# Kernel optimization log

Measured on AMD Instinct MI355X. Metric: run time of the kernel, lower is better.

## Reference

```python
import jax, jax.numpy as jnp
import numpy as np

EPS = 1e-6

def setup_inputs() -> dict:
    key = jax.random.key(0)
    k1, k2, k3, k4 = jax.random.split(key, 4)
    B, N, E, C_in, C_out = 8, 4096, 2048, 128, 128
    x = jax.random.normal(k1, (B, N, C_in), dtype=jnp.float32)
    H = jax.random.uniform(k2, (B, N, E), dtype=jnp.float32)
    # nn.Linear(in_ch, out_ch): W is [out_ch, in_ch], b is [out_ch]
    W = jax.random.normal(k3, (C_out, C_in), dtype=jnp.float32) / np.sqrt(C_in)
    b = jax.random.normal(k4, (C_out,), dtype=jnp.float32) * 0.01
    return {"x": x, "H": H, "W": W, "b": b}

def reference(x, H, W, b):
    # Degree normalizers (diag_embed + bmm in original == broadcast row scale)
    De = jnp.sum(H, axis=1) + EPS          # [B, E] hyperedge degrees
    Dv = jnp.sum(H, axis=2) + EPS          # [B, N] node degrees
    inv_sqrt_Dv = 1.0 / jnp.sqrt(Dv)       # [B, N]
    out = x * inv_sqrt_Dv[..., None]                 # Dv^{-1/2} x
    out = jnp.einsum('bne,bnc->bec', H, out)         # H^T (..)
    out = out / De[..., None]                        # De^{-1} (..)
    out = jnp.einsum('bne,bec->bnc', H, out)         # H (..)
    out = out * inv_sqrt_Dv[..., None]               # Dv^{-1/2} (..)
    return out @ W.T + b                             # Linear
```

## Files before the change

### kernel.cpp

```cpp
#include <hip/hip_runtime.h>


#define EPS 1e-6f
constexpr int B_ = 8, N_ = 4096, E_ = 2048, C_ = 128;

typedef __bf16 bf16x8 __attribute__((ext_vector_type(8)));
typedef float f32x4 __attribute__((ext_vector_type(4)));

__device__ __forceinline__ unsigned int f2bf_pack(float lo, float hi) {
  unsigned int ul = __float_as_uint(lo), uh = __float_as_uint(hi);
  ul = (ul + 0x7fffu + ((ul >> 16) & 1u)) >> 16;
  uh = (uh + 0x7fffu + ((uh >> 16) & 1u)) & 0xffff0000u;
  return uh | ul;
}

__device__ __forceinline__ void gl2lds16(const void* g, void* l) {
  __builtin_amdgcn_global_load_lds(
      (const __attribute__((address_space(1))) void*)g,
      (__attribute__((address_space(3))) void*)l, 16, 0, 0);
}

__global__ __launch_bounds__(256) void k1a_cast_dv(
    const float* __restrict__ H, unsigned short* __restrict__ Hbf,
    float* __restrict__ Dv) {
  const int t = threadIdx.x;
  const int w = t >> 6, l = t & 63;
  const size_t row = (size_t)blockIdx.x * 4 + w;
  const float* src = H + row * E_;
  unsigned short* dst = Hbf + row * E_;
  float s = 0.f;
#pragma unroll
  for (int i = 0; i < 8; ++i) {
    const f32x4 v = *(const f32x4*)(src + 256 * i + 4 * l);
    s += v[0] + v[1] + v[2] + v[3];
    uint2 p;
    p.x = f2bf_pack(v[0], v[1]);
    p.y = f2bf_pack(v[2], v[3]);
    *(uint2*)(dst + 256 * i + 4 * l) = p;
  }
#pragma unroll
  for (int o = 32; o; o >>= 1) s += __shfl_xor(s, o);
  if (l == 0) Dv[row] = s;
}

__global__ __launch_bounds__(256) void k1b_transpose_de(
    const unsigned short* __restrict__ Hbf, unsigned short* __restrict__ HT,
    float* __restrict__ De) {
  __shared__ unsigned int T[128][66];
  const int t = threadIdx.x;
  const int b = blockIdx.z;
  const int n0 = blockIdx.x * 128, e0 = blockIdx.y * 128;
  const int q = t >> 2, cq = t & 3;
  const unsigned short* r0p = Hbf + ((size_t)b * N_ + n0 + 2 * q) * E_ + e0;
  const unsigned short* r1p = r0p + E_;
#pragma unroll
  for (int i = 0; i < 8; ++i) {
    const int c = 16 * i + 4 * cq;
    const uint2 a = *(const uint2*)(r0p + c);
    const uint2 bb = *(const uint2*)(r1p + c);
    T[c + 0][q] = (a.x & 0xffffu) | (bb.x << 16);
    T[c + 1][q] = (a.x >> 16) | (bb.x & 0xffff0000u);
    T[c + 2][q] = (a.y & 0xffffu) | (bb.y << 16);
    T[c + 3][q] = (a.y >> 16) | (bb.y & 0xffff0000u);
  }
  __syncthreads();
  const int crow = t >> 1, h = t & 1;
  unsigned int u[32];
  float s = 0.f;
#pragma unroll
  for (int i = 0; i < 32; ++i) {
    u[i] = T[crow][h * 32 + i];
    s += __uint_as_float(u[i] << 16) + __uint_as_float(u[i] & 0xffff0000u);
  }
  uint4* dst = (uint4*)(HT + ((size_t)b * E_ + e0 + crow) * N_ + n0 + 64 * h);
#pragma unroll
  for (int i = 0; i < 8; ++i)
    dst[i] = make_uint4(u[4 * i], u[4 * i + 1], u[4 * i + 2], u[4 * i + 3]);
  s += __shfl_xor(s, 1);
  if (h == 0) atomicAdd(&De[b * E_ + e0 + crow], s);
}

__global__ __launch_bounds__(256) void st0_scale_transpose(
    const float* __restrict__ in, const float* __restrict__ deg,
    unsigned short* __restrict__ outT) {
  __shared__ unsigned int T[128][66];
  const int t = threadIdx.x;
  in += (size_t)blockIdx.y * N_ * 128;
  outT += (size_t)blockIdx.y * 128 * N_;
  deg += (size_t)blockIdx.y * N_;
  const int r0 = blockIdx.x * 128;
  const int q = t >> 2, cq = t & 3;
  const float* row0 = in + (size_t)(r0 + 2 * q) * 128;
  const float* row1 = row0 + 128;
  const float s0 = 1.f / sqrtf(deg[r0 + 2 * q] + EPS);
  const float s1 = 1.f / sqrtf(deg[r0 + 2 * q + 1] + EPS);
#pragma unroll
  for (int i = 0; i < 8; ++i) {
    const int c = 16 * i + 4 * cq;
    const f32x4 a = *(const f32x4*)(row0 + c);
    const f32x4 b2 = *(const f32x4*)(row1 + c);
#pragma unroll
    for (int j = 0; j < 4; ++j) T[c + j][q] = f2bf_pack(a[j] * s0, b2[j] * s1);
  }
  __syncthreads();
  const int crow = t >> 1, h = t & 1;
  unsigned int u[32];
#pragma unroll
  for (int i = 0; i < 32; ++i) u[i] = T[crow][h * 32 + i];
  uint4* dst = (uint4*)(outT + (size_t)crow * N_ + r0 + 64 * h);
#pragma unroll
  for (int i = 0; i < 8; ++i)
    dst[i] = make_uint4(u[4 * i], u[4 * i + 1], u[4 * i + 2], u[4 * i + 3]);
}

__global__ __launch_bounds__(256) void st1_sum(
    const float* __restrict__ p0, const float* __restrict__ p1,
    const float* __restrict__ De, unsigned short* __restrict__ out2T) {
  __shared__ unsigned int T[128][66];
  const int t = threadIdx.x;
  const int b = blockIdx.y;
  const int r0 = blockIdx.x * 128;
  const int q = t >> 2, cq = t & 3;
  const size_t base = ((size_t)b * E_ + r0 + 2 * q) * C_;
  const float s0 = 1.f / (De[b * E_ + r0 + 2 * q] + EPS);
  const float s1 = 1.f / (De[b * E_ + r0 + 2 * q + 1] + EPS);
#pragma unroll
  for (int i = 0; i < 8; ++i) {
    const int c = 16 * i + 4 * cq;
    const f32x4 a = *(const f32x4*)(p0 + base + c);
    const f32x4 a1 = *(const f32x4*)(p1 + base + c);
    const f32x4 bb = *(const f32x4*)(p0 + base + C_ + c);
    const f32x4 b1 = *(const f32x4*)(p1 + base + C_ + c);
#pragma unroll
    for (int j = 0; j < 4; ++j)
      T[c + j][q] = f2bf_pack((a[j] + a1[j]) * s0, (bb[j] + b1[j]) * s1);
  }
  __syncthreads();
  const int crow = t >> 1, h = t & 1;
  unsigned int u[32];
#pragma unroll
  for (int i = 0; i < 32; ++i) u[i] = T[crow][h * 32 + i];
  uint4* dst = (uint4*)(out2T + ((size_t)b * C_ + crow) * E_ + r0 + 64 * h);
#pragma unroll
  for (int i = 0; i < 8; ++i)
    dst[i] = make_uint4(u[4 * i], u[4 * i + 1], u[4 * i + 2], u[4 * i + 3]);
}

__global__ __launch_bounds__(256) void gemm_bt_splitk(
    const unsigned short* __restrict__ A, const unsigned short* __restrict__ Bt,
    float* __restrict__ C0, float* __restrict__ C1, int M, int Kfull, int Kper) {
  __shared__ unsigned short Als[128 * 32];
  __shared__ unsigned short Bls[128 * 32];
  const int t = threadIdx.x;
  const int w = t >> 6, l = t & 63;
  const int mt = blockIdx.x, sk = blockIdx.y, b = blockIdx.z;
  const unsigned short* Ab = A + ((size_t)b * M + mt * 128) * Kfull + (size_t)sk * Kper;
  const unsigned short* Btb = Bt + (size_t)b * 128 * Kfull + (size_t)sk * Kper;
  const int srow = l >> 2, scol = (l & 3) * 8;
  const unsigned short* ga0 = Ab + (size_t)(w * 32 + srow) * Kfull + scol;
  const unsigned short* ga1 = ga0 + (size_t)16 * Kfull;
  const unsigned short* gb0 = Btb + (size_t)(w * 32 + srow) * Kfull + scol;
  const unsigned short* gb1 = gb0 + (size_t)16 * Kfull;
  unsigned short* const la0 = Als + (w * 32) * 32;
  unsigned short* const la1 = Als + (w * 32 + 16) * 32;
  unsigned short* const lb0 = Bls + (w * 32) * 32;
  unsigned short* const lb1 = Bls + (w * 32 + 16) * 32;
  const int mrow = (w & 1) * 64, ncol = (w >> 1) * 64;
  const int fr = l & 15, fq = l >> 4;
  f32x4 acc[4][4];
#pragma unroll
  for (int i = 0; i < 4; ++i)
#pragma unroll
    for (int j = 0; j < 4; ++j) acc[i][j] = (f32x4){0.f, 0.f, 0.f, 0.f};
  const int nsteps = Kper / 32;
  for (int kt = 0; kt < nsteps; ++kt) {
    __syncthreads();
    gl2lds16(ga0, la0);
    gl2lds16(ga1, la1);
    gl2lds16(gb0, lb0);
    gl2lds16(gb1, lb1);
    ga0 += 32; ga1 += 32; gb0 += 32; gb1 += 32;
    __syncthreads();
    bf16x8 af[4], bfr[4];
#pragma unroll
    for (int i = 0; i < 4; ++i) {
      af[i] = *(const bf16x8*)(Als + (mrow + i * 16 + fr) * 32 + fq * 8);
      bfr[i] = *(const bf16x8*)(Bls + (ncol + i * 16 + fr) * 32 + fq * 8);
    }
#pragma unroll
    for (int i = 0; i < 4; ++i)
#pragma unroll
      for (int j = 0; j < 4; ++j)
        acc[i][j] = __builtin_amdgcn_mfma_f32_16x16x32_bf16(af[i], bfr[j], acc[i][j], 0, 0, 0);
  }
  float* Cb = (sk == 0 ? C0 : C1) + ((size_t)b * M + mt * 128) * 128;
#pragma unroll
  for (int i = 0; i < 4; ++i)
#pragma unroll
    for (int j = 0; j < 4; ++j)
#pragma unroll
      for (int r = 0; r < 4; ++r) {
        const int row = mrow + i * 16 + fq * 4 + r;
        const int col = ncol + j * 16 + fr;
        Cb[(size_t)row * 128 + col] = acc[i][j][r];
      }
}

__global__ __launch_bounds__(256) void k5_linear(
    float* __restrict__ io, const float* __restrict__ q1,
    const float* __restrict__ W, const float* __restrict__ bias,
    const float* __restrict__ Dv) {
  __shared__ unsigned short Als[128 * 136];
  __shared__ unsigned short Wls[128 * 136];
  const int t = threadIdx.x;
  const size_t r0 = (size_t)blockIdx.x * 128;
  {
    const int row = t >> 1, h = t & 1;
    const float* src0 = io + (r0 + row) * 128 + h * 64;
    const float* src1 = q1 + (r0 + row) * 128 + h * 64;
    const float sc = 1.f / sqrtf(Dv[r0 + row] + EPS);
    unsigned short* ld = Als + row * 136 + h * 64;
    const float* wsrc = W + row * 128 + h * 64;
    unsigned short* lw = Wls + row * 136 + h * 64;
#pragma unroll
    for (int i = 0; i < 16; ++i) {
      const f32x4 a = *(const f32x4*)(src0 + 4 * i);
      const f32x4 a1 = *(const f32x4*)(src1 + 4 * i);
      uint2 p;
      p.x = f2bf_pack((a[0] + a1[0]) * sc, (a[1] + a1[1]) * sc);
      p.y = f2bf_pack((a[2] + a1[2]) * sc, (a[3] + a1[3]) * sc);
      *(uint2*)(ld + 4 * i) = p;
      const f32x4 ww = *(const f32x4*)(wsrc + 4 * i);
      uint2 pw;
      pw.x = f2bf_pack(ww[0], ww[1]);
      pw.y = f2bf_pack(ww[2], ww[3]);
      *(uint2*)(lw + 4 * i) = pw;
    }
  }
  __syncthreads();
  const int w = t >> 6, l = t & 63;
  const int mrow = (w & 1) * 64, ncol = (w >> 1) * 64;
  const int fr = l & 15, fq = l >> 4;
  f32x4 acc[4][4];
#pragma unroll
  for (int i = 0; i < 4; ++i)
#pragma unroll
    for (int j = 0; j < 4; ++j) acc[i][j] = (f32x4){0.f, 0.f, 0.f, 0.f};
#pragma unroll
  for (int s = 0; s < 4; ++s) {
    bf16x8 af[4], bfr[4];
#pragma unroll
    for (int i = 0; i < 4; ++i) {
      af[i] = *(const bf16x8*)(Als + (mrow + i * 16 + fr) * 136 + s * 32 + fq * 8);
      bfr[i] = *(const bf16x8*)(Wls + (ncol + i * 16 + fr) * 136 + s * 32 + fq * 8);
    }
#pragma unroll
    for (int i = 0; i < 4; ++i)
#pragma unroll
      for (int j = 0; j < 4; ++j)
        acc[i][j] = __builtin_amdgcn_mfma_f32_16x16x32_bf16(af[i], bfr[j], acc[i][j], 0, 0, 0);
  }
#pragma unroll
  for (int i = 0; i < 4; ++i)
#pragma unroll
    for (int j = 0; j < 4; ++j)
#pragma unroll
      for (int r = 0; r < 4; ++r) {
        const int row = mrow + i * 16 + fq * 4 + r;
        const int col = ncol + j * 16 + fr;
        io[(r0 + row) * 128 + col] = acc[i][j][r] + bias[col];
      }
}

extern "C" void kernel_launch(void* const* d_in, const int* in_sizes, int n_in,
                              void* d_out, int out_size, void* d_ws, size_t ws_size,
                              hipStream_t stream) {
  const float* x = (const float*)d_in[0];
  const float* H = (const float*)d_in[1];
  const float* W = (const float*)d_in[2];
  const float* bias = (const float*)d_in[3];
  float* out = (float*)d_out;

  unsigned short* Hbf = (unsigned short*)d_ws;
  unsigned short* HT = Hbf + (size_t)B_ * N_ * E_;
  unsigned short* xsT = HT + (size_t)B_ * N_ * E_;
  unsigned short* out2T = xsT + (size_t)B_ * C_ * N_;
  float* Dv = (float*)(out2T + (size_t)B_ * C_ * E_);
  float* De = Dv + B_ * N_;

  float* g1p0 = out;
  float* g1p1 = out + (size_t)B_ * E_ * C_;
  float* g2p1 = (float*)HT;

  hipMemsetAsync(De, 0, (size_t)B_ * E_ * sizeof(float), stream);

  k1a_cast_dv<<<dim3(B_ * N_ / 4), 256, 0, stream>>>(H, Hbf, Dv);
  k1b_transpose_de<<<dim3(N_ / 128, E_ / 128, B_), 256, 0, stream>>>(Hbf, HT, De);
  st0_scale_transpose<<<dim3(N_ / 128, B_), 256, 0, stream>>>(x, Dv, xsT);
  gemm_bt_splitk<<<dim3(E_ / 128, 2, B_), 256, 0, stream>>>(HT, xsT, g1p0, g1p1, E_, N_, N_ / 2);
  st1_sum<<<dim3(E_ / 128, B_), 256, 0, stream>>>(g1p0, g1p1, De, out2T);
  gemm_bt_splitk<<<dim3(N_ / 128, 2, B_), 256, 0, stream>>>(Hbf, out2T, out, g2p1, N_, E_, E_ / 2);
  k5_linear<<<dim3(B_ * N_ / 128), 256, 0, stream>>>(out, g2p1, W, bias, Dv);
}
```

Baseline: 592.5 us.

## Eliminate H transpose pass, fuse De into cast, use 4-way split-K

Drops the separate transpose of the bf16 H matrix and its buffer. The first GEMM now reads row-major Hbf directly and transposes tiles in registers into swizzled LDS, while the column sums De are accumulated during the initial cast kernel. Both GEMMs move from 2-way to 4-way split-K with extra partial buffers that are reduced in the follow-up kernels. This saves a full read and write of the large H copy, at the cost of more partial-sum traffic and a less efficient B-tile load path in gemm1.

```diff
diff --git a/kernel.cpp b/kernel.cpp
--- a/kernel.cpp
+++ b/kernel.cpp
@@ -20,64 +20,51 @@
       (__attribute__((address_space(3))) void*)l, 16, 0, 0);
 }
 
-__global__ __launch_bounds__(256) void k1a_cast_dv(
+__global__ __launch_bounds__(256) void k1_fused(
     const float* __restrict__ H, unsigned short* __restrict__ Hbf,
-    float* __restrict__ Dv) {
+    float* __restrict__ Dv, float* __restrict__ De) {
+  __shared__ float Lde[4][2048];
   const int t = threadIdx.x;
   const int w = t >> 6, l = t & 63;
-  const size_t row = (size_t)blockIdx.x * 4 + w;
-  const float* src = H + row * E_;
-  unsigned short* dst = Hbf + row * E_;
-  float s = 0.f;
-#pragma unroll
-  for (int i = 0; i < 8; ++i) {
-    const f32x4 v = *(const f32x4*)(src + 256 * i + 4 * l);
-    s += v[0] + v[1] + v[2] + v[3];
-    uint2 p;
-    p.x = f2bf_pack(v[0], v[1]);
-    p.y = f2bf_pack(v[2], v[3]);
-    *(uint2*)(dst + 256 * i + 4 * l) = p;
-  }
-#pragma unroll
-  for (int o = 32; o; o >>= 1) s += __shfl_xor(s, o);
-  if (l == 0) Dv[row] = s;
-}
-
-__global__ __launch_bounds__(256) void k1b_transpose_de(
-    const unsigned short* __restrict__ Hbf, unsigned short* __restrict__ HT,
-    float* __restrict__ De) {
-  __shared__ unsigned int T[128][66];
-  const int t = threadIdx.x;
-  const int b = blockIdx.z;
-  const int n0 = blockIdx.x * 128, e0 = blockIdx.y * 128;
-  const int q = t >> 2, cq = t & 3;
-  const unsigned short* r0p = Hbf + ((size_t)b * N_ + n0 + 2 * q) * E_ + e0;
-  const unsigned short* r1p = r0p + E_;
-#pragma unroll
-  for (int i = 0; i < 8; ++i) {
-    const int c = 16 * i + 4 * cq;
-    const uint2 a = *(const uint2*)(r0p + c);
-    const uint2 bb = *(const uint2*)(r1p + c);
-    T[c + 0][q] = (a.x & 0xffffu) | (bb.x << 16);
-    T[c + 1][q] = (a.x >> 16) | (bb.x & 0xffff0000u);
-    T[c + 2][q] = (a.y & 0xffffu) | (bb.y << 16);
-    T[c + 3][q] = (a.y >> 16) | (bb.y & 0xffff0000u);
-  }
+  const size_t row0 = (size_t)blockIdx.x * 64;
+  const int b = (int)(row0 >> 12);
+  f32x4 dc[8];
+#pragma unroll
+  for (int j = 0; j < 8; ++j) dc[j] = (f32x4){0.f, 0.f, 0.f, 0.f};
+  for (int i = 0; i < 16; ++i) {
+    const size_t r = row0 + w * 16 + i;
+    const float* src = H + r * E_;
+    unsigned short* dst = Hbf + r * E_;
+    float rs = 0.f;
+#pragma unroll
+    for (int j = 0; j < 8; ++j) {
+      const f32x4 v = *(const f32x4*)(src + 256 * j + 4 * l);
+      dc[j] += v;
+      rs += v[0] + v[1] + v[2] + v[3];
+      uint2 p;
+      p.x = f2bf_pack(v[0], v[1]);
+      p.y = f2bf_pack(v[2], v[3]);
+      *(uint2*)(dst + 256 * j + 4 * l) = p;
+    }
+#pragma unroll
+    for (int o = 32; o; o >>= 1) rs += __shfl_xor(rs, o);
+    if (l == 0) Dv[r] = rs;
+  }
+#pragma unroll
+  for (int j = 0; j < 8; ++j) *(f32x4*)&Lde[w][256 * j + 4 * l] = dc[j];
   __syncthreads();
-  const int crow = t >> 1, h = t & 1;
-  unsigned int u[32];
-  float s = 0.f;
-#pragma unroll
-  for (int i = 0; i < 32; ++i) {
-    u[i] = T[crow][h * 32 + i];
-    s += __uint_as_float(u[i] << 16) + __uint_as_float(u[i] & 0xffff0000u);
-  }
-  uint4* dst = (uint4*)(HT + ((size_t)b * E_ + e0 + crow) * N_ + n0 + 64 * h);
-#pragma unroll
-  for (int i = 0; i < 8; ++i)
-    dst[i] = make_uint4(u[4 * i], u[4 * i + 1], u[4 * i + 2], u[4 * i + 3]);
-  s += __shfl_xor(s, 1);
-  if (h == 0) atomicAdd(&De[b * E_ + e0 + crow], s);
+  const int c0 = t * 8;
+  f32x4 s0 = (f32x4){0.f, 0.f, 0.f, 0.f}, s1 = s0;
+#pragma unroll
+  for (int ww = 0; ww < 4; ++ww) {
+    s0 += *(const f32x4*)&Lde[ww][c0];
+    s1 += *(const f32x4*)&Lde[ww][c0 + 4];
+  }
+  float* dp = De + b * E_ + c0;
+#pragma unroll
+  for (int j = 0; j < 4; ++j) atomicAdd(dp + j, s0[j]);
+#pragma unroll
+  for (int j = 0; j < 4; ++j) atomicAdd(dp + 4 + j, s1[j]);
 }
 
 __global__ __launch_bounds__(256) void st0_scale_transpose(
@@ -113,42 +100,111 @@
     dst[i] = make_uint4(u[4 * i], u[4 * i + 1], u[4 * i + 2], u[4 * i + 3]);
 }
 
-__global__ __launch_bounds__(256) void st1_sum(
-    const float* __restrict__ p0, const float* __restrict__ p1,
-    const float* __restrict__ De, unsigned short* __restrict__ out2T) {
-  __shared__ unsigned int T[128][66];
-  const int t = threadIdx.x;
-  const int b = blockIdx.y;
-  const int r0 = blockIdx.x * 128;
-  const int q = t >> 2, cq = t & 3;
-  const size_t base = ((size_t)b * E_ + r0 + 2 * q) * C_;
-  const float s0 = 1.f / (De[b * E_ + r0 + 2 * q] + EPS);
-  const float s1 = 1.f / (De[b * E_ + r0 + 2 * q + 1] + EPS);
-#pragma unroll
-  for (int i = 0; i < 8; ++i) {
-    const int c = 16 * i + 4 * cq;
-    const f32x4 a = *(const f32x4*)(p0 + base + c);
-    const f32x4 a1 = *(const f32x4*)(p1 + base + c);
-    const f32x4 bb = *(const f32x4*)(p0 + base + C_ + c);
-    const f32x4 b1 = *(const f32x4*)(p1 + base + C_ + c);
+__global__ __launch_bounds__(256) void gemm1_tr(
+    const unsigned short* __restrict__ Hbf, const unsigned short* __restrict__ xsT,
+    float* __restrict__ P) {
+  __shared__ unsigned short Als[128 * 32];
+  __shared__ unsigned short Bls[128 * 40];
+  const int t = threadIdx.x;
+  const int w = t >> 6, l = t & 63;
+  const int et = blockIdx.x, sk = blockIdx.y, b = blockIdx.z;
+  const int k0 = sk * (N_ / 4);
+  const int e0 = et * 128;
+  const unsigned short* Ab = xsT + (size_t)b * C_ * N_ + k0;
+  const int srow = l >> 2, scol = (l & 3) * 8;
+  const unsigned short* ga0 = Ab + (size_t)(w * 32 + srow) * N_ + scol;
+  const unsigned short* ga1 = ga0 + (size_t)16 * N_;
+  unsigned short* const la0 = Als + (w * 32) * 32;
+  unsigned short* const la1 = Als + (w * 32 + 16) * 32;
+  const int np = t >> 4, q = t & 15;
+  const int sw = (q & 3) << 3;
+  const unsigned short* gb = Hbf + (size_t)b * N_ * E_ + (size_t)(k0 + 2 * np) * E_ + e0 + 8 * q;
+  const int mrow = (w & 1) * 64, ncol = (w >> 1) * 64;
+  const int fr = l & 15, fq = l >> 4;
+  f32x4 acc[4][4];
+#pragma unroll
+  for (int i = 0; i < 4; ++i)
+#pragma unroll
+    for (int j = 0; j < 4; ++j) acc[i][j] = (f32x4){0.f, 0.f, 0.f, 0.f};
+  uint4 pl = *(const uint4*)gb;
+  uint4 ph = *(const uint4*)(gb + E_);
+  const int nsteps = (N_ / 4) / 32;
+  for (int kt = 0; kt < nsteps; ++kt) {
+    __syncthreads();
+    gl2lds16(ga0, la0);
+    gl2lds16(ga1, la1);
+    ga0 += 32;
+    ga1 += 32;
+    {
+      unsigned int wl[4] = {pl.x, pl.y, pl.z, pl.w};
+      unsigned int wh[4] = {ph.x, ph.y, ph.z, ph.w};
+#pragma unroll
+      for (int j = 0; j < 8; ++j) {
+        const unsigned int lo16 = (wl[j >> 1] >> (16 * (j & 1))) & 0xffffu;
+        const unsigned int hi16 = (wh[j >> 1] >> (16 * (j & 1))) & 0xffffu;
+        *(unsigned int*)(Bls + (8 * q + j) * 40 + ((2 * np) ^ sw)) = lo16 | (hi16 << 16);
+      }
+    }
+    if (kt + 1 < nsteps) {
+      const unsigned short* g2 = gb + (size_t)(kt + 1) * 32 * E_;
+      pl = *(const uint4*)g2;
+      ph = *(const uint4*)(g2 + E_);
+    }
+    __syncthreads();
+    bf16x8 af[4], bfr[4];
+#pragma unroll
+    for (int i = 0; i < 4; ++i) {
+      af[i] = *(const bf16x8*)(Als + (mrow + i * 16 + fr) * 32 + fq * 8);
+      const int brow = ncol + i * 16 + fr;
+      const int nsw = (fq * 8) ^ (((brow >> 3) & 3) << 3);
+      bfr[i] = *(const bf16x8*)(Bls + brow * 40 + nsw);
+    }
+#pragma unroll
+    for (int i = 0; i < 4; ++i)
+#pragma unroll
+      for (int j = 0; j < 4; ++j)
+        acc[i][j] = __builtin_amdgcn_mfma_f32_16x16x32_bf16(af[i], bfr[j], acc[i][j], 0, 0, 0);
+  }
+  float* Pb = P + (((size_t)sk * B_ + b) * C_) * E_ + e0;
+#pragma unroll
+  for (int i = 0; i < 4; ++i)
 #pragma unroll
     for (int j = 0; j < 4; ++j)
-      T[c + j][q] = f2bf_pack((a[j] + a1[j]) * s0, (bb[j] + b1[j]) * s1);
-  }
-  __syncthreads();
-  const int crow = t >> 1, h = t & 1;
-  unsigned int u[32];
-#pragma unroll
-  for (int i = 0; i < 32; ++i) u[i] = T[crow][h * 32 + i];
-  uint4* dst = (uint4*)(out2T + ((size_t)b * C_ + crow) * E_ + r0 + 64 * h);
-#pragma unroll
-  for (int i = 0; i < 8; ++i)
-    dst[i] = make_uint4(u[4 * i], u[4 * i + 1], u[4 * i + 2], u[4 * i + 3]);
-}
-
-__global__ __launch_bounds__(256) void gemm_bt_splitk(
+#pragma unroll
+      for (int r = 0; r < 4; ++r) {
+        const int row = mrow + i * 16 + fq * 4 + r;
+        const int col = ncol + j * 16 + fr;
+        Pb[(size_t)row * E_ + col] = acc[i][j][r];
+      }
+}
+
+__global__ __launch_bounds__(256) void st1_sum4(
+    const float* __restrict__ P, const float* __restrict__ De,
+    unsigned short* __restrict__ out2T) {
+  const size_t SP = (size_t)B_ * C_ * E_;
+  const size_t idx = ((size_t)blockIdx.x * 256 + threadIdx.x) * 8;
+  const int e = (int)(idx & (E_ - 1));
+  const int b = (int)(idx >> 18);
+  f32x4 s0 = (f32x4){0.f, 0.f, 0.f, 0.f}, s1 = s0;
+#pragma unroll
+  for (int s = 0; s < 4; ++s) {
+    s0 += *(const f32x4*)(P + s * SP + idx);
+    s1 += *(const f32x4*)(P + s * SP + idx + 4);
+  }
+  const f32x4 d0 = *(const f32x4*)(De + b * E_ + e);
+  const f32x4 d1 = *(const f32x4*)(De + b * E_ + e + 4);
+  uint4 o;
+  o.x = f2bf_pack(s0[0] / (d0[0] + EPS), s0[1] / (d0[1] + EPS));
+  o.y = f2bf_pack(s0[2] / (d0[2] + EPS), s0[3] / (d0[3] + EPS));
+  o.z = f2bf_pack(s1[0] / (d1[0] + EPS), s1[1] / (d1[1] + EPS));
+  o.w = f2bf_pack(s1[2] / (d1[2] + EPS), s1[3] / (d1[3] + EPS));
+  *(uint4*)(out2T + idx) = o;
+}
+
+__global__ __launch_bounds__(256) void gemm_bt_splitk4(
     const unsigned short* __restrict__ A, const unsigned short* __restrict__ Bt,
-    float* __restrict__ C0, float* __restrict__ C1, int M, int Kfull, int Kper) {
+    float* __restrict__ Q0, float* __restrict__ Q1, float* __restrict__ Q2,
+    float* __restrict__ Q3, int M, int Kfull, int Kper) {
   __shared__ unsigned short Als[128 * 32];
   __shared__ unsigned short Bls[128 * 32];
   const int t = threadIdx.x;
@@ -193,7 +249,8 @@
       for (int j = 0; j < 4; ++j)
         acc[i][j] = __builtin_amdgcn_mfma_f32_16x16x32_bf16(af[i], bfr[j], acc[i][j], 0, 0, 0);
   }
-  float* Cb = (sk == 0 ? C0 : C1) + ((size_t)b * M + mt * 128) * 128;
+  float* Q = (sk == 0) ? Q0 : (sk == 1) ? Q1 : (sk == 2) ? Q2 : Q3;
+  float* Cb = Q + ((size_t)b * M + mt * 128) * 128;
 #pragma unroll
   for (int i = 0; i < 4; ++i)
 #pragma unroll
@@ -206,8 +263,9 @@
       }
 }
 
-__global__ __launch_bounds__(256) void k5_linear(
+__global__ __launch_bounds__(256) void k5_linear4(
     float* __restrict__ io, const float* __restrict__ q1,
+    const float* __restrict__ q2, const float* __restrict__ q3,
     const float* __restrict__ W, const float* __restrict__ bias,
     const float* __restrict__ Dv) {
   __shared__ unsigned short Als[128 * 136];
@@ -216,19 +274,20 @@
   const size_t r0 = (size_t)blockIdx.x * 128;
   {
     const int row = t >> 1, h = t & 1;
-    const float* src0 = io + (r0 + row) * 128 + h * 64;
-    const float* src1 = q1 + (r0 + row) * 128 + h * 64;
+    const size_t off = (r0 + row) * 128 + h * 64;
     const float sc = 1.f / sqrtf(Dv[r0 + row] + EPS);
     unsigned short* ld = Als + row * 136 + h * 64;
     const float* wsrc = W + row * 128 + h * 64;
     unsigned short* lw = Wls + row * 136 + h * 64;
 #pragma unroll
     for (int i = 0; i < 16; ++i) {
-      const f32x4 a = *(const f32x4*)(src0 + 4 * i);
-      const f32x4 a1 = *(const f32x4*)(src1 + 4 * i);
+      f32x4 a = *(const f32x4*)(io + off + 4 * i);
+      a += *(const f32x4*)(q1 + off + 4 * i);
+      a += *(const f32x4*)(q2 + off + 4 * i);
+      a += *(const f32x4*)(q3 + off + 4 * i);
       uint2 p;
-      p.x = f2bf_pack((a[0] + a1[0]) * sc, (a[1] + a1[1]) * sc);
-      p.y = f2bf_pack((a[2] + a1[2]) * sc, (a[3] + a1[3]) * sc);
+      p.x = f2bf_pack(a[0] * sc, a[1] * sc);
+      p.y = f2bf_pack(a[2] * sc, a[3] * sc);
       *(uint2*)(ld + 4 * i) = p;
       const f32x4 ww = *(const f32x4*)(wsrc + 4 * i);
       uint2 pw;
@@ -282,23 +341,24 @@
   float* out = (float*)d_out;
 
   unsigned short* Hbf = (unsigned short*)d_ws;
-  unsigned short* HT = Hbf + (size_t)B_ * N_ * E_;
-  unsigned short* xsT = HT + (size_t)B_ * N_ * E_;
+  unsigned short* xsT = Hbf + (size_t)B_ * N_ * E_;
   unsigned short* out2T = xsT + (size_t)B_ * C_ * N_;
-  float* Dv = (float*)(out2T + (size_t)B_ * C_ * E_);
+  float* P = (float*)(out2T + (size_t)B_ * C_ * E_);
+  float* Q123 = P + 4 * (size_t)B_ * C_ * E_;
+  float* Dv = Q123 + 3 * (size_t)B_ * N_ * C_;
   float* De = Dv + B_ * N_;
 
-  float* g1p0 = out;
-  float* g1p1 = out + (size_t)B_ * E_ * C_;
-  float* g2p1 = (float*)HT;
+  float* q1 = Q123;
+  float* q2 = Q123 + (size_t)B_ * N_ * C_;
+  float* q3 = Q123 + 2 * (size_t)B_ * N_ * C_;
 
   hipMemsetAsync(De, 0, (size_t)B_ * E_ * sizeof(float), stream);
 
-  k1a_cast_dv<<<dim3(B_ * N_ / 4), 256, 0, stream>>>(H, Hbf, Dv);
-  k1b_transpose_de<<<dim3(N_ / 128, E_ / 128, B_), 256, 0, stream>>>(Hbf, HT, De);
+  k1_fused<<<dim3(B_ * N_ / 64), 256, 0, stream>>>(H, Hbf, Dv, De);
   st0_scale_transpose<<<dim3(N_ / 128, B_), 256, 0, stream>>>(x, Dv, xsT);
-  gemm_bt_splitk<<<dim3(E_ / 128, 2, B_), 256, 0, stream>>>(HT, xsT, g1p0, g1p1, E_, N_, N_ / 2);
-  st1_sum<<<dim3(E_ / 128, B_), 256, 0, stream>>>(g1p0, g1p1, De, out2T);
-  gemm_bt_splitk<<<dim3(N_ / 128, 2, B_), 256, 0, stream>>>(Hbf, out2T, out, g2p1, N_, E_, E_ / 2);
-  k5_linear<<<dim3(B_ * N_ / 128), 256, 0, stream>>>(out, g2p1, W, bias, Dv);
-}
+  gemm1_tr<<<dim3(E_ / 128, 4, B_), 256, 0, stream>>>(Hbf, xsT, P);
+  st1_sum4<<<dim3(B_ * C_ * E_ / 8 / 256), 256, 0, stream>>>(P, De, out2T);
+  gemm_bt_splitk4<<<dim3(N_ / 128, 4, B_), 256, 0, stream>>>(
+      Hbf, out2T, out, q1, q2, q3, N_, E_, E_ / 4);
+  k5_linear4<<<dim3(B_ * N_ / 128), 256, 0, stream>>>(out, q1, q2, q3, W, bias, Dv);
+}
```

Measured after the change: 557.6 us. -5.9%, faster.
